# Optimization experiments

Measured on AMD Instinct MI355X. Metric: run time of the kernel, lower is better.

## Reference

```python
import jax, jax.numpy as jnp
import numpy as np

DIM = 1024
NUM_HEADS = 8
HEAD_DIM = 64
INNER = NUM_HEADS * HEAD_DIM  # 512


def setup_inputs() -> dict:
    key = jax.random.key(0)
    ks = jax.random.split(key, 7)
    B, N, M = 8, 512, 4096
    x = jax.random.normal(ks[0], (B, N, DIM), dtype=jnp.float32)
    context = jax.random.normal(ks[1], (B, M, DIM), dtype=jnp.float32)
    s_in = 1.0 / np.sqrt(DIM)
    s_inner = 1.0 / np.sqrt(INNER)
    # Linear weights stored as [in, out] for x @ W
    Wq = jax.random.normal(ks[2], (DIM, INNER), dtype=jnp.float32) * s_in
    Wk = jax.random.normal(ks[3], (DIM, INNER), dtype=jnp.float32) * s_in
    Wv = jax.random.normal(ks[4], (DIM, INNER), dtype=jnp.float32) * s_in
    Wo = jax.random.normal(ks[5], (INNER, DIM), dtype=jnp.float32) * s_inner
    bo = jax.random.normal(ks[6], (DIM,), dtype=jnp.float32) * 0.01
    return {"x": x, "context": context, "Wq": Wq, "Wk": Wk, "Wv": Wv, "Wo": Wo, "bo": bo}


def reference(x, context, Wq, Wk, Wv, Wo, bo):
    B, N, _ = x.shape
    M = context.shape[1]
    scale = HEAD_DIM ** -0.5
    # project and split heads: [B, H, N, D]
    q = (x @ Wq).reshape(B, N, NUM_HEADS, HEAD_DIM).transpose(0, 2, 1, 3)
    k = (context @ Wk).reshape(B, M, NUM_HEADS, HEAD_DIM).transpose(0, 2, 1, 3)
    v = (context @ Wv).reshape(B, M, NUM_HEADS, HEAD_DIM).transpose(0, 2, 1, 3)
    # full attention matrix [B, H, N, M] as in the original module
    attn = jax.nn.softmax(jnp.einsum('bhnd,bhmd->bhnm', q, k) * scale, axis=-1)
    out = jnp.einsum('bhnm,bhmd->bhnd', attn, v)  # [B, H, N, D]
    out = out.transpose(0, 2, 1, 3).reshape(B, N, INNER)
    return out @ Wo + bo
```

## Files before the change

kernel.cpp:

```cpp
#include <hip/hip_runtime.h>
#include <hip/hip_bf16.h>

#define B_SZ 8
#define N_Q 512
#define M_KV 4096
#define DIM 1024
#define INNER 512
#define NHEADS 8
#define HDIM 64

typedef __attribute__((ext_vector_type(4))) float floatx4;
typedef __attribute__((ext_vector_type(8))) short shortx8;
typedef __attribute__((ext_vector_type(4))) short shortx4;

#define QSCALE 0.18033688011112042f

__device__ inline unsigned short f2bf(float f) {
  union { float f; unsigned u; } x; x.f = f;
  unsigned r = x.u + 0x7FFFu + ((x.u >> 16) & 1u);
  return (unsigned short)(r >> 16);
}

__device__ inline shortx8 cvt8(floatx4 a, floatx4 b) {
  shortx8 h;
  h[0] = (short)f2bf(a[0]); h[1] = (short)f2bf(a[1]);
  h[2] = (short)f2bf(a[2]); h[3] = (short)f2bf(a[3]);
  h[4] = (short)f2bf(b[0]); h[5] = (short)f2bf(b[1]);
  h[6] = (short)f2bf(b[2]); h[7] = (short)f2bf(b[3]);
  return h;
}

__device__ inline void gload16(const void* g, void* l) {
  __builtin_amdgcn_global_load_lds(
      (const __attribute__((address_space(1))) void*)g,
      (__attribute__((address_space(3))) void*)l, 16, 0, 0);
}

__global__ void k_cvt_bf16(const float* __restrict__ src,
                           unsigned short* __restrict__ dst, long n) {
  long stride = (long)gridDim.x * 256 * 8;
  for (long i = ((long)blockIdx.x * 256 + threadIdx.x) * 8; i < n; i += stride) {
    floatx4 a = *reinterpret_cast<const floatx4*>(src + i);
    floatx4 b = *reinterpret_cast<const floatx4*>(src + i + 4);
    *reinterpret_cast<shortx8*>(dst + i) = cvt8(a, b);
  }
}

__global__ void k_transpose_all(const float* __restrict__ Wq,
                                const float* __restrict__ Wk,
                                const float* __restrict__ Wv,
                                const float* __restrict__ Wo,
                                unsigned short* __restrict__ Wqt,
                                unsigned short* __restrict__ Wkvt,
                                unsigned short* __restrict__ Wot) {
  __shared__ unsigned short t[32][36];
  const int z = blockIdx.z;
  const float* W;
  unsigned short* Wt;
  int K, N;
  if (z == 0)      { W = Wq; Wt = Wqt;  K = 1024; N = 512; }
  else if (z == 1) { W = Wk; Wt = Wkvt; K = 1024; N = 512; }
  else if (z == 2) { W = Wv; Wt = Wkvt + (size_t)512 * 1024; K = 1024; N = 512; }
  else             { W = Wo; Wt = Wot;  K = 512;  N = 1024; }
  if ((int)blockIdx.x * 32 >= K || (int)blockIdx.y * 32 >= N) return;
  const int kt = blockIdx.x * 32, nt = blockIdx.y * 32;
  const int tr = threadIdx.x >> 3;
  const int tc = (threadIdx.x & 7) * 4;
  floatx4 v = *reinterpret_cast<const floatx4*>(&W[(long)(kt + tr) * N + nt + tc]);
  #pragma unroll
  for (int j = 0; j < 4; ++j) t[tr][tc + j] = f2bf(v[j]);
  __syncthreads();
  shortx4 o;
  #pragma unroll
  for (int j = 0; j < 4; ++j) o[j] = (short)t[tc + j][tr];
  *reinterpret_cast<shortx4*>(&Wt[(long)(nt + tr) * K + kt + tc]) = o;
}

__global__ __launch_bounds__(256, 4)
void k_gemm_kv(const unsigned short* __restrict__ Ah,
               const unsigned short* __restrict__ Wkvt,
               unsigned short* __restrict__ Kh,
               unsigned short* __restrict__ Vt) {
  __shared__ unsigned short As[2][128 * 32];
  __shared__ unsigned short Bs[2][128 * 32];
  const int tid = threadIdx.x;
  const int lane = tid & 63;
  const int w = tid >> 6;
  const int wr = w >> 1, wc = w & 1;
  const int fr = lane & 15, fc = lane >> 4;

  const int L = ((blockIdx.x & 7) << 8) + (blockIdx.x >> 3);
  const int mt = L >> 3, nt = L & 7;
  const long arow0 = (long)mt << 7;
  const long bcol0 = (long)nt << 7;

  const int grow = lane >> 2;
  const int gpos = lane & 3;

  floatx4 acc[4][4] = {};

  #define STAGE(buf, kt)                                                      \
    {                                                                         \
      _Pragma("unroll")                                                       \
      for (int g = 0; g < 2; ++g) {                                           \
        const int rl = w * 32 + g * 16 + grow;                                \
        const int cc = gpos ^ ((rl >> 1) & 3);                                \
        gload16(Ah + (arow0 + rl) * 1024 + (kt) + cc * 8,                     \
                &As[buf][(w * 32 + g * 16) * 32]);                            \
        gload16(Wkvt + (bcol0 + rl) * 1024 + (kt) + cc * 8,                   \
                &Bs[buf][(w * 32 + g * 16) * 32]);                            \
      }                                                                       \
    }

  STAGE(0, 0);
  __syncthreads();

  for (int i = 0; i < 32; ++i) {
    const int cur = i & 1;
    if (i < 31) STAGE(cur ^ 1, (i + 1) << 5);

    shortx8 af[4], bf[4];
    #pragma unroll
    for (int rb = 0; rb < 4; ++rb) {
      int row = wr * 64 + rb * 16 + fr;
      af[rb] = *reinterpret_cast<const shortx8*>(
          &As[cur][row * 32 + ((fc ^ ((row >> 1) & 3)) * 8)]);
    }
    #pragma unroll
    for (int cb = 0; cb < 4; ++cb) {
      int row = wc * 64 + cb * 16 + fr;
      bf[cb] = *reinterpret_cast<const shortx8*>(
          &Bs[cur][row * 32 + ((fc ^ ((row >> 1) & 3)) * 8)]);
    }
    __builtin_amdgcn_s_setprio(1);
    #pragma unroll
    for (int rb = 0; rb < 4; ++rb) {
      #pragma unroll
      for (int cb = 0; cb < 4; ++cb)
        acc[rb][cb] = __builtin_amdgcn_mfma_f32_16x16x32_bf16(
            af[rb], bf[cb], acc[rb][cb], 0, 0, 0);
    }
    __builtin_amdgcn_s_setprio(0);
    __syncthreads();
  }
  #undef STAGE

  #pragma unroll
  for (int rb = 0; rb < 4; ++rb) {
    #pragma unroll
    for (int cb = 0; cb < 4; ++cb) {
      long gr0 = arow0 + wr * 64 + rb * 16 + fc * 4;
      long gc = bcol0 + wc * 64 + cb * 16 + fr;
      long b = gr0 >> 12, m = gr0 & 4095;
      if (gc < 512) {
        long h = gc >> 6, d = gc & 63;
        #pragma unroll
        for (int r = 0; r < 4; ++r)
          Kh[((((b * 8 + h) << 12) + m + r) << 6) + d] = f2bf(acc[rb][cb][r]);
      } else {
        long h = (gc - 512) >> 6, d = (gc - 512) & 63;
        shortx4 hv;
        #pragma unroll
        for (int r = 0; r < 4; ++r) hv[r] = (short)f2bf(acc[rb][cb][r]);
        *reinterpret_cast<shortx4*>(&Vt[(((b * 8 + h) * 64 + d) << 12) + m]) = hv;
      }
    }
  }
}

__global__ __launch_bounds__(256, 4)
void k_qproj(const float* __restrict__ x,
             const unsigned short* __restrict__ Wqt,
             unsigned short* __restrict__ Qh) {
  __shared__ unsigned short As[2][4096];
  __shared__ unsigned short Bs[2][4096];
  const int tid = threadIdx.x;
  const int lane = tid & 63;
  const int w = tid >> 6;
  const int wr = w >> 1, wc = w & 1;
  const int fr = lane & 15, fc = lane >> 4;

  const int L = ((blockIdx.x & 7) << 4) + (blockIdx.x >> 3);
  const long arow0 = (long)(L >> 2) << 7;
  const long bcol0 = (long)(L & 3) << 7;

  const int grow = lane >> 2;
  const int gpos = lane & 3;
  const int arw = tid >> 1;
  const int ahalf = tid & 1;
  const int aswz = (arw >> 1) & 3;
  const int as0 = ((2 * ahalf) ^ aswz) * 8;
  const int as1 = ((2 * ahalf + 1) ^ aswz) * 8;

  floatx4 acc[4][4] = {};

  #define STAGE_B(buf, kt)                                                    \
    { _Pragma("unroll")                                                       \
      for (int g = 0; g < 2; ++g) {                                           \
        const int rl = w * 32 + g * 16 + grow;                                \
        const int cc = gpos ^ ((rl >> 1) & 3);                                \
        gload16(Wqt + (bcol0 + rl) * 1024 + (kt) + cc * 8,                    \
                &Bs[buf][(w * 32 + g * 16) * 32]);                            \
      } }

  {
    const float* s = x + (arow0 + arw) * 1024 + ahalf * 16;
    floatx4 a0 = *reinterpret_cast<const floatx4*>(s);
    floatx4 a1 = *reinterpret_cast<const floatx4*>(s + 4);
    floatx4 a2 = *reinterpret_cast<const floatx4*>(s + 8);
    floatx4 a3 = *reinterpret_cast<const floatx4*>(s + 12);
    STAGE_B(0, 0);
    *reinterpret_cast<shortx8*>(&As[0][arw * 32 + as0]) = cvt8(a0, a1);
    *reinterpret_cast<shortx8*>(&As[0][arw * 32 + as1]) = cvt8(a2, a3);
  }
  __syncthreads();

  for (int i = 0; i < 32; ++i) {
    const int cur = i & 1;
    const bool more = i < 31;
    floatx4 a0, a1, a2, a3;
    if (more) {
      const int ktn = (i + 1) << 5;
      const float* s = x + (arow0 + arw) * 1024 + ktn + ahalf * 16;
      a0 = *reinterpret_cast<const floatx4*>(s);
      a1 = *reinterpret_cast<const floatx4*>(s + 4);
      a2 = *reinterpret_cast<const floatx4*>(s + 8);
      a3 = *reinterpret_cast<const floatx4*>(s + 12);
      STAGE_B(cur ^ 1, ktn);
    }

    shortx8 af[4], bf[4];
    #pragma unroll
    for (int rb = 0; rb < 4; ++rb) {
      int row = wr * 64 + rb * 16 + fr;
      af[rb] = *reinterpret_cast<const shortx8*>(
          &As[cur][row * 32 + ((fc ^ ((row >> 1) & 3)) * 8)]);
    }
    #pragma unroll
    for (int cb = 0; cb < 4; ++cb) {
      int row = wc * 64 + cb * 16 + fr;
      bf[cb] = *reinterpret_cast<const shortx8*>(
          &Bs[cur][row * 32 + ((fc ^ ((row >> 1) & 3)) * 8)]);
    }
    __builtin_amdgcn_s_setprio(1);
    #pragma unroll
    for (int rb = 0; rb < 4; ++rb) {
      #pragma unroll
      for (int cb = 0; cb < 4; ++cb)
        acc[rb][cb] = __builtin_amdgcn_mfma_f32_16x16x32_bf16(
            af[rb], bf[cb], acc[rb][cb], 0, 0, 0);
    }
    __builtin_amdgcn_s_setprio(0);

    if (more) {
      *reinterpret_cast<shortx8*>(&As[cur ^ 1][arw * 32 + as0]) = cvt8(a0, a1);
      *reinterpret_cast<shortx8*>(&As[cur ^ 1][arw * 32 + as1]) = cvt8(a2, a3);
    }
    __syncthreads();
  }
  #undef STAGE_B

  #pragma unroll
  for (int rb = 0; rb < 4; ++rb) {
    #pragma unroll
    for (int cb = 0; cb < 4; ++cb) {
      long gr0 = arow0 + wr * 64 + rb * 16 + fc * 4;
      long gc = bcol0 + wc * 64 + cb * 16 + fr;
      long b = gr0 >> 9, m = gr0 & 511;
      long h = gc >> 6, d = gc & 63;
      #pragma unroll
      for (int r = 0; r < 4; ++r)
        Qh[((((b * 8 + h) << 9) + m + r) << 6) + d] =
            f2bf(acc[rb][cb][r] * QSCALE);
    }
  }
}

__global__ __launch_bounds__(256, 4)
void k_out(const unsigned short* __restrict__ Aat,
           const unsigned short* __restrict__ Wot,
           float* __restrict__ out, const float* __restrict__ bias) {
  __shared__ unsigned short As[2][4096];
  __shared__ unsigned short Bs[2][4096];
  const int tid = threadIdx.x;
  const int lane = tid & 63;
  const int w = tid >> 6;
  const int wr = w >> 1, wc = w & 1;
  const int fr = lane & 15, fc = lane >> 4;

  const int L = ((blockIdx.x & 7) << 5) + (blockIdx.x >> 3);
  const long arow0 = (long)(L >> 3) << 7;
  const long bcol0 = (long)(L & 7) << 7;

  const int grow = lane >> 2;
  const int gpos = lane & 3;

  floatx4 acc[4][4] = {};

  #define STAGE2(buf, kt)                                                     \
    { _Pragma("unroll")                                                       \
      for (int g = 0; g < 2; ++g) {                                           \
        const int rl = w * 32 + g * 16 + grow;                                \
        const int cc = gpos ^ ((rl >> 1) & 3);                                \
        gload16(Aat + (arow0 + rl) * 512 + (kt) + cc * 8,                     \
                &As[buf][(w * 32 + g * 16) * 32]);                            \
        gload16(Wot + (bcol0 + rl) * 512 + (kt) + cc * 8,                     \
                &Bs[buf][(w * 32 + g * 16) * 32]);                            \
      } }

  STAGE2(0, 0);
  __syncthreads();

  for (int i = 0; i < 16; ++i) {
    const int cur = i & 1;
    if (i < 15) STAGE2(cur ^ 1, (i + 1) << 5);

    shortx8 af[4], bf[4];
    #pragma unroll
    for (int rb = 0; rb < 4; ++rb) {
      int row = wr * 64 + rb * 16 + fr;
      af[rb] = *reinterpret_cast<const shortx8*>(
          &As[cur][row * 32 + ((fc ^ ((row >> 1) & 3)) * 8)]);
    }
    #pragma unroll
    for (int cb = 0; cb < 4; ++cb) {
      int row = wc * 64 + cb * 16 + fr;
      bf[cb] = *reinterpret_cast<const shortx8*>(
          &Bs[cur][row * 32 + ((fc ^ ((row >> 1) & 3)) * 8)]);
    }
    __builtin_amdgcn_s_setprio(1);
    #pragma unroll
    for (int rb = 0; rb < 4; ++rb) {
      #pragma unroll
      for (int cb = 0; cb < 4; ++cb)
        acc[rb][cb] = __builtin_amdgcn_mfma_f32_16x16x32_bf16(
            af[rb], bf[cb], acc[rb][cb], 0, 0, 0);
    }
    __builtin_amdgcn_s_setprio(0);
    __syncthreads();
  }
  #undef STAGE2

  #pragma unroll
  for (int rb = 0; rb < 4; ++rb) {
    #pragma unroll
    for (int cb = 0; cb < 4; ++cb) {
      long gr0 = arow0 + wr * 64 + rb * 16 + fc * 4;
      long gc = bcol0 + wc * 64 + cb * 16 + fr;
      float bv = bias[gc];
      #pragma unroll
      for (int r = 0; r < 4; ++r)
        out[(gr0 + r) * 1024 + gc] = acc[rb][cb][r] + bv;
    }
  }
}

__global__ __launch_bounds__(256, 3)
void k_attn(const unsigned short* __restrict__ Qh,
            const unsigned short* __restrict__ Kh,
            const unsigned short* __restrict__ Vt,
            float* __restrict__ Opart, float* __restrict__ Lpart) {
  __shared__ unsigned short Ks[2][64 * 64];
  __shared__ unsigned short Vs[2][64 * 64];
  __shared__ unsigned short QPs[128 * 72];
  const int tid = threadIdx.x;
  const int lane = tid & 63;
  const int w = tid >> 6;
  const int wg = blockIdx.x;
  const int bh = wg & 63;
  const int qt = (wg >> 6) & 3;
  const int sp = wg >> 8;
  const int fr = lane & 15, fc = lane >> 4;

  const unsigned short* Qbase = Qh + (((long)bh << 9) + qt * 128) * 64;
  const unsigned short* Kbase = Kh + (((long)bh) << 18);
  const unsigned short* Vbase = Vt + (((long)bh) << 18);

  const int grow = lane >> 3;
  const int gpos = lane & 7;

  #define STAGE_KV(buf, mt_)                                              \
    { _Pragma("unroll")                                                   \
      for (int j = 0; j < 2; ++j) {                                       \
        const int r = w * 16 + j * 8 + grow;                              \
        const int c = gpos ^ (r & 7);                                     \
        gload16(Kbase + ((mt_) * 64 + r) * 64 + c * 8,                    \
                &Ks[buf][(w * 16 + j * 8) * 64]);                         \
        gload16(Vbase + (((long)r) << 12) + (mt_) * 64 + c * 8,           \
                &Vs[buf][(w * 16 + j * 8) * 64]);                         \
      } }

  const int mt0 = sp * 16;
  {
    #pragma unroll
    for (int j = 0; j < 4; ++j) {
      const int r = w * 32 + j * 8 + grow;
      const int c = gpos ^ (r & 7);
      gload16(Qbase + r * 64 + c * 8, &QPs[(w * 32 + j * 8) * 64]);
    }
    STAGE_KV(0, mt0);
  }
  __syncthreads();

  shortx8 qf[2][2];
  #pragma unroll
  for (int qb = 0; qb < 2; ++qb) {
    const int row = w * 32 + qb * 16 + fr;
    #pragma unroll
    for (int kk = 0; kk < 2; ++kk)
      qf[qb][kk] = *reinterpret_cast<const shortx8*>(
          &QPs[row * 64 + (((kk * 4 + fc) ^ (row & 7)) * 8)]);
  }
  __syncthreads();

  floatx4 o_acc[2][4] = {};
  float lql[2] = {0.f, 0.f};

  for (int it = 0; it < 16; ++it) {
    const int cur = it & 1;
    if (it < 15) STAGE_KV(cur ^ 1, mt0 + it + 1);

    floatx4 s[2][4];
    __builtin_amdgcn_s_setprio(1);
    #pragma unroll
    for (int mb = 0; mb < 4; ++mb) {
      const int krow = mb * 16 + fr;
      shortx8 k0 = *reinterpret_cast<const shortx8*>(
          &Ks[cur][krow * 64 + ((fc ^ (fr & 7)) * 8)]);
      shortx8 k1 = *reinterpret_cast<const shortx8*>(
          &Ks[cur][krow * 64 + (((4 + fc) ^ (fr & 7)) * 8)]);
      #pragma unroll
      for (int qb = 0; qb < 2; ++qb) {
        floatx4 z = {};
        z = __builtin_amdgcn_mfma_f32_16x16x32_bf16(k0, qf[qb][0], z, 0, 0, 0);
        s[qb][mb] = __builtin_amdgcn_mfma_f32_16x16x32_bf16(
            k1, qf[qb][1], z, 0, 0, 0);
      }
    }
    __builtin_amdgcn_s_setprio(0);

    #pragma unroll
    for (int qb = 0; qb < 2; ++qb) {
      #pragma unroll
      for (int mb = 0; mb < 4; ++mb) {
        shortx4 pk;
        #pragma unroll
        for (int r = 0; r < 4; ++r) {
          float pv = exp2f(s[qb][mb][r]);
          lql[qb] += pv;
          pk[r] = (short)f2bf(pv);
        }
        *reinterpret_cast<shortx4*>(
            &QPs[(w * 32 + qb * 16 + fr) * 72 + mb * 16 + fc * 4]) = pk;
      }
    }

    __builtin_amdgcn_s_setprio(1);
    #pragma unroll
    for (int kk = 0; kk < 2; ++kk) {
      shortx8 pf[2];
      #pragma unroll
      for (int qb = 0; qb < 2; ++qb)
        pf[qb] = *reinterpret_cast<const shortx8*>(
            &QPs[(w * 32 + qb * 16 + fr) * 72 + kk * 32 + fc * 8]);
      #pragma unroll
      for (int db = 0; db < 4; ++db) {
        const int vrow = db * 16 + fr;
        shortx8 vf = *reinterpret_cast<const shortx8*>(
            &Vs[cur][vrow * 64 + (((kk * 4 + fc) ^ (fr & 7)) * 8)]);
        #pragma unroll
        for (int qb = 0; qb < 2; ++qb)
          o_acc[qb][db] = __builtin_amdgcn_mfma_f32_16x16x32_bf16(
              pf[qb], vf, o_acc[qb][db], 0, 0, 0);
      }
    }
    __builtin_amdgcn_s_setprio(0);
    __syncthreads();
  }
  #undef STAGE_KV

  #pragma unroll
  for (int qb = 0; qb < 2; ++qb) {
    float l = lql[qb];
    l += __shfl_xor(l, 16);
    l += __shfl_xor(l, 32);
    if (fc == 0) Lpart[(long)wg * 128 + w * 32 + qb * 16 + fr] = l;
  }
  float* Ob = Opart + (long)wg * 8192;
  #pragma unroll
  for (int qb = 0; qb < 2; ++qb) {
    #pragma unroll
    for (int r = 0; r < 4; ++r) {
      const int prow = w * 32 + qb * 16 + fc * 4 + r;
      #pragma unroll
      for (int db = 0; db < 4; ++db)
        Ob[prow * 64 + db * 16 + fr] = o_acc[qb][db][r];
    }
  }
}

__global__ void k_attn_reduce(const float* __restrict__ Opart,
                              const float* __restrict__ Lpart,
                              unsigned short* __restrict__ Aat) {
  const int tid = threadIdx.x;
  const int g = blockIdx.x * 4 + (tid >> 6);
  const int d = tid & 63;
  const int bh = g >> 9, n = g & 511;
  const int b = bh >> 3, h = bh & 7;
  const int qt = n >> 7, rr = n & 127;
  float o = 0.f, l = 0.f;
  #pragma unroll
  for (int p = 0; p < 4; ++p) {
    const long wgp = ((p * 4 + qt) << 6) + bh;
    o += Opart[wgp * 8192 + rr * 64 + d];
    l += Lpart[wgp * 128 + rr];
  }
  Aat[((long)(b * 512 + n)) * 512 + h * 64 + d] = f2bf(o / l);
}

extern "C" void kernel_launch(void* const* d_in, const int* in_sizes, int n_in,
                              void* d_out, int out_size, void* d_ws, size_t ws_size,
                              hipStream_t stream) {
  const float* x   = (const float*)d_in[0];
  const float* ctx = (const float*)d_in[1];
  const float* Wq  = (const float*)d_in[2];
  const float* Wk  = (const float*)d_in[3];
  const float* Wv  = (const float*)d_in[4];
  const float* Wo  = (const float*)d_in[5];
  const float* bo  = (const float*)d_in[6];
  float* out = (float*)d_out;

  char* ws = (char*)d_ws;
  unsigned short* Qh   = (unsigned short*)(ws);
  unsigned short* Kh   = (unsigned short*)(ws + (4ull  << 20));
  unsigned short* Vt   = (unsigned short*)(ws + (36ull << 20));
  unsigned short* ctxh = (unsigned short*)(ws + (68ull << 20));
  unsigned short* Aat  = (unsigned short*)(ws + (68ull << 20));
  float*          Opart= (float*)         (ws + (76ull << 20));
  float*          Lpart= (float*)         (ws + (110ull << 20));
  unsigned short* Wqt  = (unsigned short*)(ws + (132ull << 20));
  unsigned short* Wkvt = (unsigned short*)(ws + (133ull << 20));
  unsigned short* Wot  = (unsigned short*)(ws + (135ull << 20));

  k_cvt_bf16<<<dim3(2048), dim3(256), 0, stream>>>(
      ctx, ctxh, (long)B_SZ * M_KV * DIM);

  k_transpose_all<<<dim3(32, 32, 4), dim3(256), 0, stream>>>(
      Wq, Wk, Wv, Wo, Wqt, Wkvt, Wot);

  k_qproj<<<dim3(128), dim3(256), 0, stream>>>(x, Wqt, Qh);
  k_gemm_kv<<<dim3(2048), dim3(256), 0, stream>>>(ctxh, Wkvt, Kh, Vt);

  k_attn<<<dim3(1024), dim3(256), 0, stream>>>(Qh, Kh, Vt, Opart, Lpart);
  k_attn_reduce<<<dim3(8192), dim3(256), 0, stream>>>(Opart, Lpart, Aat);

  k_out<<<dim3(256), dim3(256), 0, stream>>>(Aat, Wot, out, bo);
}
```

Measured before the change: 248.8 us.

## Fuse context fp32-to-bf16 conversion into KV GEMM loads and transpose score MFMA

Removes the separate context conversion kernel. The KV projection GEMM now stages fp32 context tiles directly into LDS and converts them to bf16 in registers with packed cvt instructions. This drops one full write and one full read of the 64MB-scale bf16 context copy, at the cost of doubling the A-tile LDS footprint and lowering occupancy to 3 blocks. The attention kernel also swaps the QK^T MFMA operand order, so P is written to LDS as scalar stores and row sums are reduced across a different lane dimension.

```diff
diff --git a/kernel.cpp b/kernel.cpp
--- a/kernel.cpp
+++ b/kernel.cpp
@@ -30,20 +30,19 @@
   return h;
 }
 
+__device__ inline shortx8 pk8(floatx4 a, floatx4 b) {
+  union { unsigned u[4]; shortx8 s; } p;
+  asm("v_cvt_pk_bf16_f32 %0, %1, %2" : "=v"(p.u[0]) : "v"(a[0]), "v"(a[1]));
+  asm("v_cvt_pk_bf16_f32 %0, %1, %2" : "=v"(p.u[1]) : "v"(a[2]), "v"(a[3]));
+  asm("v_cvt_pk_bf16_f32 %0, %1, %2" : "=v"(p.u[2]) : "v"(b[0]), "v"(b[1]));
+  asm("v_cvt_pk_bf16_f32 %0, %1, %2" : "=v"(p.u[3]) : "v"(b[2]), "v"(b[3]));
+  return p.s;
+}
+
 __device__ inline void gload16(const void* g, void* l) {
   __builtin_amdgcn_global_load_lds(
       (const __attribute__((address_space(1))) void*)g,
       (__attribute__((address_space(3))) void*)l, 16, 0, 0);
-}
-
-__global__ void k_cvt_bf16(const float* __restrict__ src,
-                           unsigned short* __restrict__ dst, long n) {
-  long stride = (long)gridDim.x * 256 * 8;
-  for (long i = ((long)blockIdx.x * 256 + threadIdx.x) * 8; i < n; i += stride) {
-    floatx4 a = *reinterpret_cast<const floatx4*>(src + i);
-    floatx4 b = *reinterpret_cast<const floatx4*>(src + i + 4);
-    *reinterpret_cast<shortx8*>(dst + i) = cvt8(a, b);
-  }
 }
 
 __global__ void k_transpose_all(const float* __restrict__ Wq,
@@ -76,12 +75,12 @@
   *reinterpret_cast<shortx4*>(&Wt[(long)(nt + tr) * K + kt + tc]) = o;
 }
 
-__global__ __launch_bounds__(256, 4)
-void k_gemm_kv(const unsigned short* __restrict__ Ah,
+__global__ __launch_bounds__(256, 3)
+void k_gemm_kv(const float* __restrict__ Af,
                const unsigned short* __restrict__ Wkvt,
                unsigned short* __restrict__ Kh,
                unsigned short* __restrict__ Vt) {
-  __shared__ unsigned short As[2][128 * 32];
+  __shared__ float As[2][128 * 32];
   __shared__ unsigned short Bs[2][128 * 32];
   const int tid = threadIdx.x;
   const int lane = tid & 63;
@@ -94,21 +93,28 @@
   const long arow0 = (long)mt << 7;
   const long bcol0 = (long)nt << 7;
 
-  const int grow = lane >> 2;
-  const int gpos = lane & 3;
+  const int ga_row = lane >> 3;
+  const int ga_pos = lane & 7;
+  const int gb_row = lane >> 2;
+  const int gb_pos = lane & 3;
 
   floatx4 acc[4][4] = {};
 
   #define STAGE(buf, kt)                                                      \
     {                                                                         \
       _Pragma("unroll")                                                       \
-      for (int g = 0; g < 2; ++g) {                                           \
-        const int rl = w * 32 + g * 16 + grow;                                \
-        const int cc = gpos ^ ((rl >> 1) & 3);                                \
-        gload16(Ah + (arow0 + rl) * 1024 + (kt) + cc * 8,                     \
-                &As[buf][(w * 32 + g * 16) * 32]);                            \
-        gload16(Wkvt + (bcol0 + rl) * 1024 + (kt) + cc * 8,                   \
-                &Bs[buf][(w * 32 + g * 16) * 32]);                            \
+      for (int j = 0; j < 4; ++j) {                                           \
+        const int rA = w * 32 + j * 8 + ga_row;                               \
+        const int cA = ga_pos ^ (rA & 7);                                     \
+        gload16(Af + (arow0 + rA) * 1024 + (kt) + cA * 4,                     \
+                &As[buf][(w * 32 + j * 8) * 32]);                             \
+      }                                                                       \
+      _Pragma("unroll")                                                       \
+      for (int j = 0; j < 2; ++j) {                                           \
+        const int rB = w * 32 + j * 16 + gb_row;                              \
+        const int cB = gb_pos ^ ((rB >> 1) & 3);                              \
+        gload16(Wkvt + (bcol0 + rB) * 1024 + (kt) + cB * 8,                   \
+                &Bs[buf][(w * 32 + j * 16) * 32]);                            \
       }                                                                       \
     }
 
@@ -122,13 +128,16 @@
     shortx8 af[4], bf[4];
     #pragma unroll
     for (int rb = 0; rb < 4; ++rb) {
-      int row = wr * 64 + rb * 16 + fr;
-      af[rb] = *reinterpret_cast<const shortx8*>(
-          &As[cur][row * 32 + ((fc ^ ((row >> 1) & 3)) * 8)]);
-    }
-    #pragma unroll
-    for (int cb = 0; cb < 4; ++cb) {
-      int row = wc * 64 + cb * 16 + fr;
+      const int row = wr * 64 + rb * 16 + fr;
+      const int s = row & 7;
+      const float* base = &As[cur][row * 32];
+      floatx4 f0 = *reinterpret_cast<const floatx4*>(base + (((2 * fc) ^ s) << 2));
+      floatx4 f1 = *reinterpret_cast<const floatx4*>(base + (((2 * fc + 1) ^ s) << 2));
+      af[rb] = pk8(f0, f1);
+    }
+    #pragma unroll
+    for (int cb = 0; cb < 4; ++cb) {
+      const int row = wc * 64 + cb * 16 + fr;
       bf[cb] = *reinterpret_cast<const shortx8*>(
           &Bs[cur][row * 32 + ((fc ^ ((row >> 1) & 3)) * 8)]);
     }
@@ -404,17 +413,17 @@
 
   shortx8 qf[2][2];
   #pragma unroll
-  for (int qb = 0; qb < 2; ++qb) {
-    const int row = w * 32 + qb * 16 + fr;
+  for (int rf = 0; rf < 2; ++rf) {
+    const int row = w * 32 + rf * 16 + fr;
     #pragma unroll
     for (int kk = 0; kk < 2; ++kk)
-      qf[qb][kk] = *reinterpret_cast<const shortx8*>(
+      qf[rf][kk] = *reinterpret_cast<const shortx8*>(
           &QPs[row * 64 + (((kk * 4 + fc) ^ (row & 7)) * 8)]);
   }
   __syncthreads();
 
   floatx4 o_acc[2][4] = {};
-  float lql[2] = {0.f, 0.f};
+  float l_part[2][4] = {};
 
   for (int it = 0; it < 16; ++it) {
     const int cur = it & 1;
@@ -423,35 +432,32 @@
     floatx4 s[2][4];
     __builtin_amdgcn_s_setprio(1);
     #pragma unroll
-    for (int mb = 0; mb < 4; ++mb) {
-      const int krow = mb * 16 + fr;
+    for (int cb = 0; cb < 4; ++cb) {
+      const int krow = cb * 16 + fr;
       shortx8 k0 = *reinterpret_cast<const shortx8*>(
           &Ks[cur][krow * 64 + ((fc ^ (fr & 7)) * 8)]);
       shortx8 k1 = *reinterpret_cast<const shortx8*>(
           &Ks[cur][krow * 64 + (((4 + fc) ^ (fr & 7)) * 8)]);
       #pragma unroll
-      for (int qb = 0; qb < 2; ++qb) {
+      for (int rf = 0; rf < 2; ++rf) {
         floatx4 z = {};
-        z = __builtin_amdgcn_mfma_f32_16x16x32_bf16(k0, qf[qb][0], z, 0, 0, 0);
-        s[qb][mb] = __builtin_amdgcn_mfma_f32_16x16x32_bf16(
-            k1, qf[qb][1], z, 0, 0, 0);
+        z = __builtin_amdgcn_mfma_f32_16x16x32_bf16(qf[rf][0], k0, z, 0, 0, 0);
+        s[rf][cb] = __builtin_amdgcn_mfma_f32_16x16x32_bf16(
+            qf[rf][1], k1, z, 0, 0, 0);
       }
     }
     __builtin_amdgcn_s_setprio(0);
 
     #pragma unroll
-    for (int qb = 0; qb < 2; ++qb) {
-      #pragma unroll
-      for (int mb = 0; mb < 4; ++mb) {
-        shortx4 pk;
+    for (int rf = 0; rf < 2; ++rf) {
+      #pragma unroll
+      for (int cb = 0; cb < 4; ++cb) {
         #pragma unroll
         for (int r = 0; r < 4; ++r) {
-          float pv = exp2f(s[qb][mb][r]);
-          lql[qb] += pv;
-          pk[r] = (short)f2bf(pv);
+          float pv = exp2f(s[rf][cb][r]);
+          l_part[rf][r] += pv;
+          QPs[(w * 32 + rf * 16 + fc * 4 + r) * 72 + cb * 16 + fr] = f2bf(pv);
         }
-        *reinterpret_cast<shortx4*>(
-            &QPs[(w * 32 + qb * 16 + fr) * 72 + mb * 16 + fc * 4]) = pk;
       }
     }
 
@@ -460,18 +466,18 @@
     for (int kk = 0; kk < 2; ++kk) {
       shortx8 pf[2];
       #pragma unroll
-      for (int qb = 0; qb < 2; ++qb)
-        pf[qb] = *reinterpret_cast<const shortx8*>(
-            &QPs[(w * 32 + qb * 16 + fr) * 72 + kk * 32 + fc * 8]);
+      for (int rf = 0; rf < 2; ++rf)
+        pf[rf] = *reinterpret_cast<const shortx8*>(
+            &QPs[(w * 32 + rf * 16 + fr) * 72 + kk * 32 + fc * 8]);
       #pragma unroll
       for (int db = 0; db < 4; ++db) {
         const int vrow = db * 16 + fr;
         shortx8 vf = *reinterpret_cast<const shortx8*>(
             &Vs[cur][vrow * 64 + (((kk * 4 + fc) ^ (fr & 7)) * 8)]);
         #pragma unroll
-        for (int qb = 0; qb < 2; ++qb)
-          o_acc[qb][db] = __builtin_amdgcn_mfma_f32_16x16x32_bf16(
-              pf[qb], vf, o_acc[qb][db], 0, 0, 0);
+        for (int rf = 0; rf < 2; ++rf)
+          o_acc[rf][db] = __builtin_amdgcn_mfma_f32_16x16x32_bf16(
+              pf[rf], vf, o_acc[rf][db], 0, 0, 0);
       }
     }
     __builtin_amdgcn_s_setprio(0);
@@ -479,22 +485,21 @@
   }
   #undef STAGE_KV
 
-  #pragma unroll
-  for (int qb = 0; qb < 2; ++qb) {
-    float l = lql[qb];
-    l += __shfl_xor(l, 16);
-    l += __shfl_xor(l, 32);
-    if (fc == 0) Lpart[(long)wg * 128 + w * 32 + qb * 16 + fr] = l;
-  }
   float* Ob = Opart + (long)wg * 8192;
   #pragma unroll
-  for (int qb = 0; qb < 2; ++qb) {
+  for (int rf = 0; rf < 2; ++rf) {
     #pragma unroll
     for (int r = 0; r < 4; ++r) {
-      const int prow = w * 32 + qb * 16 + fc * 4 + r;
+      float l = l_part[rf][r];
+      l += __shfl_xor(l, 1);
+      l += __shfl_xor(l, 2);
+      l += __shfl_xor(l, 4);
+      l += __shfl_xor(l, 8);
+      const int prow = w * 32 + rf * 16 + fc * 4 + r;
+      if (fr == 0) Lpart[(long)wg * 128 + prow] = l;
       #pragma unroll
       for (int db = 0; db < 4; ++db)
-        Ob[prow * 64 + db * 16 + fr] = o_acc[qb][db][r];
+        Ob[prow * 64 + db * 16 + fr] = o_acc[rf][db][r];
     }
   }
 }
@@ -534,7 +539,6 @@
   unsigned short* Qh   = (unsigned short*)(ws);
   unsigned short* Kh   = (unsigned short*)(ws + (4ull  << 20));
   unsigned short* Vt   = (unsigned short*)(ws + (36ull << 20));
-  unsigned short* ctxh = (unsigned short*)(ws + (68ull << 20));
   unsigned short* Aat  = (unsigned short*)(ws + (68ull << 20));
   float*          Opart= (float*)         (ws + (76ull << 20));
   float*          Lpart= (float*)         (ws + (110ull << 20));
@@ -542,14 +546,12 @@
   unsigned short* Wkvt = (unsigned short*)(ws + (133ull << 20));
   unsigned short* Wot  = (unsigned short*)(ws + (135ull << 20));
 
-  k_cvt_bf16<<<dim3(2048), dim3(256), 0, stream>>>(
-      ctx, ctxh, (long)B_SZ * M_KV * DIM);
-
   k_transpose_all<<<dim3(32, 32, 4), dim3(256), 0, stream>>>(
       Wq, Wk, Wv, Wo, Wqt, Wkvt, Wot);
 
   k_qproj<<<dim3(128), dim3(256), 0, stream>>>(x, Wqt, Qh);
-  k_gemm_kv<<<dim3(2048), dim3(256), 0, stream>>>(ctxh, Wkvt, Kh, Vt);
+
+  k_gemm_kv<<<dim3(2048), dim3(256), 0, stream>>>(ctx, Wkvt, Kh, Vt);
 
   k_attn<<<dim3(1024), dim3(256), 0, stream>>>(Qh, Kh, Vt, Opart, Lpart);
   k_attn_reduce<<<dim3(8192), dim3(256), 0, stream>>>(Opart, Lpart, Aat);
```

New measurement: 268.5 us. 7.9% more time.
